# Optimization experiments

Measured on AMD Instinct MI355X. Metric: run time of the kernel, lower is better.

## Reference

```python
import jax, jax.numpy as jnp
import numpy as np

B, S, QD, VD, H = 32, 2048, 1024, 1024, 1024
NEG = -1e9


def setup_inputs() -> dict:
    key = jax.random.key(0)
    ks = jax.random.split(key, 7)
    query = jax.random.normal(ks[0], (B, QD), dtype=jnp.float32)
    value = jax.random.normal(ks[1], (B, S, VD), dtype=jnp.float32)
    mask = jax.random.randint(ks[2], (B, S), 0, 2).astype(bool)
    # params (Linear weights stored as [in, out] for einsum convenience)
    Wq = jax.random.normal(ks[3], (QD, H), dtype=jnp.float32) / np.sqrt(QD)
    bq = jax.random.normal(ks[4], (H,), dtype=jnp.float32) * 0.01
    Wv = jax.random.normal(ks[5], (VD, H), dtype=jnp.float32) / np.sqrt(VD)
    w = jax.random.normal(ks[6], (H,), dtype=jnp.float32) / np.sqrt(H)
    return {"query": query, "value": value, "mask": mask,
            "Wq": Wq, "bq": bq, "Wv": Wv, "w": w}


def reference(query, value, mask, Wq, bq, Wv, w):
    # q-projection: [B, H]
    hq = query @ Wq + bq
    # v-projection: [B, S, H]
    hv = jnp.einsum('bsv,vh->bsh', value, Wv)
    # additive attention energies: [B, S]
    logits = jnp.einsum('bsh,h->bs', jnp.tanh(hq[:, None, :] + hv), w)
    logits = jnp.where(mask, logits, NEG)
    return jax.nn.softmax(logits, axis=-1)
```

## Files before the change

### kernel.cpp

```cpp
#include <hip/hip_runtime.h>
#include <hip/hip_bf16.h>
#include <hip/hip_fp16.h>

typedef _Float16 f16;
typedef _Float16 f16x8 __attribute__((ext_vector_type(8)));
typedef float f32x16 __attribute__((ext_vector_type(16)));
typedef unsigned int u32;

#define BB 32
#define SS 2048
#define HH 1024
#define KK 1024

#define WS_BP 0
#define WS_HQ (2u*1024u*1024u)
#define WS_LP (WS_HQ + 131072u)

__device__ __forceinline__ float tanh_f(float x) {
    float e = __expf(2.0f * x);
    return 1.0f - 2.0f * __builtin_amdgcn_rcpf(e + 1.0f);
}

__device__ __forceinline__ void write_a16(char* dst, int off, float4 va, float4 vb) {
    union { f16 h[8]; uint4 u; } pk;
    pk.h[0] = (f16)va.x; pk.h[1] = (f16)va.y; pk.h[2] = (f16)va.z; pk.h[3] = (f16)va.w;
    pk.h[4] = (f16)vb.x; pk.h[5] = (f16)vb.y; pk.h[6] = (f16)vb.z; pk.h[7] = (f16)vb.w;
    *(uint4*)(dst + off) = pk.u;
}

__global__ void pack_wv(const float* __restrict__ Wv, f16* __restrict__ BP) {
    int i = blockIdx.x * 256 + threadIdx.x;
    int k = i >> 10, n = i & 1023;
    float v = Wv[i];
    int ntb = n >> 8, wc = (n >> 6) & 3, ntl = (n >> 5) & 1, nl = n & 31;
    int kit = k >> 5, ks = (k >> 4) & 1, lg = (k >> 3) & 1, j = k & 7;
    int lane = lg * 32 + nl;
    BP[((((((ntb * 32 + kit) * 4 + wc) * 2 + ks) * 2 + ntl) * 64 + lane) * 8) + j] = (f16)v;
}

__global__ void hq_kernel(const float* __restrict__ query, const float* __restrict__ Wq,
                          const float* __restrict__ bq, float* __restrict__ hq) {
    int b = blockIdx.y;
    int h = (blockIdx.x & 3) * 256 + threadIdx.x;
    int v0 = (blockIdx.x >> 2) * 256;
    float acc = 0.f;
#pragma unroll 8
    for (int v = 0; v < 256; ++v)
        acc += query[b * 1024 + v0 + v] * Wq[(v0 + v) * 1024 + h];
    if (v0 == 0) acc += bq[h];
    atomicAdd(&hq[b * 1024 + h], acc);
}

__launch_bounds__(256, 3)
__global__ void fused_main(const float* __restrict__ value, const f16* __restrict__ BP,
                           const float* __restrict__ hq, const float* __restrict__ wvec,
                           float* __restrict__ lpart) {
    __shared__ char A0[4096];
    __shared__ char A1[4096];
    __shared__ float part[256];

    int bid = blockIdx.x;
    int tile = (bid & 7) * 512 + (bid >> 3);
    int Mt = tile >> 2, ntb = tile & 3;
    int m0 = Mt << 6;
    int b = m0 >> 11, s0 = m0 & 2047;

    int tid = threadIdx.x;
    int wc = tid >> 6, l = tid & 63;
    int l31 = l & 31, lg = l >> 5;

    int arow = tid >> 2;
    const float* aga = value + (size_t)(m0 + arow) * 1024 + (tid & 3) * 8;
    int aw = ((arow >> 5) * 2 + ((tid & 3) >> 1)) * 1024
           + ((((tid & 3) & 1) << 5) + (arow & 31)) * 16;

    const char* bg = (const char*)BP + (size_t)ntb * 524288 + (size_t)wc * 4096
                   + (size_t)l * 16;

    int a_off0 = l * 16;
    int a_off1 = 2048 + l * 16;

    const f32x16 fzero = {};
    f32x16 acc[2][2];
#pragma unroll
    for (int mt = 0; mt < 2; ++mt)
#pragma unroll
        for (int nt = 0; nt < 2; ++nt) acc[mt][nt] = fzero;

    f16x8 bvA[4], bvB[4];
    float4 fe0, fe1, fo0, fo1;

#define COMPUTE(Ab, BV) do { \
        f16x8 a00 = *(const f16x8*)((Ab) + a_off0); \
        f16x8 a10 = *(const f16x8*)((Ab) + a_off1); \
        f16x8 a01 = *(const f16x8*)((Ab) + a_off0 + 1024); \
        f16x8 a11 = *(const f16x8*)((Ab) + a_off1 + 1024); \
        __builtin_amdgcn_s_setprio(1); \
        acc[0][0] = __builtin_amdgcn_mfma_f32_32x32x16_f16(a00, (BV)[0], acc[0][0], 0, 0, 0); \
        acc[0][1] = __builtin_amdgcn_mfma_f32_32x32x16_f16(a00, (BV)[1], acc[0][1], 0, 0, 0); \
        acc[1][0] = __builtin_amdgcn_mfma_f32_32x32x16_f16(a10, (BV)[0], acc[1][0], 0, 0, 0); \
        acc[1][1] = __builtin_amdgcn_mfma_f32_32x32x16_f16(a10, (BV)[1], acc[1][1], 0, 0, 0); \
        acc[0][0] = __builtin_amdgcn_mfma_f32_32x32x16_f16(a01, (BV)[2], acc[0][0], 0, 0, 0); \
        acc[0][1] = __builtin_amdgcn_mfma_f32_32x32x16_f16(a01, (BV)[3], acc[0][1], 0, 0, 0); \
        acc[1][0] = __builtin_amdgcn_mfma_f32_32x32x16_f16(a11, (BV)[2], acc[1][0], 0, 0, 0); \
        acc[1][1] = __builtin_amdgcn_mfma_f32_32x32x16_f16(a11, (BV)[3], acc[1][1], 0, 0, 0); \
        __builtin_amdgcn_s_setprio(0); \
    } while (0)

#define LOADB(BV, e) do { \
        const char* bt_ = bg + (size_t)(e) * 16384; \
        (BV)[0] = *(const f16x8*)(bt_); \
        (BV)[1] = *(const f16x8*)(bt_ + 1024); \
        (BV)[2] = *(const f16x8*)(bt_ + 2048); \
        (BV)[3] = *(const f16x8*)(bt_ + 3072); \
    } while (0)

    {
        const float4* ap = (const float4*)aga;
        float4 p0 = ap[0], p1 = ap[1];
        write_a16(A0, aw, p0, p1);
        const float4* ap1 = (const float4*)(aga + 32);
        fo0 = ap1[0]; fo1 = ap1[1];
        LOADB(bvA, 0);
        asm volatile("s_waitcnt lgkmcnt(0)" ::: "memory");
        __builtin_amdgcn_s_barrier();
    }

#pragma unroll 1
    for (int tt = 0; tt < 16; ++tt) {
        {
            LOADB(bvB, 2 * tt + 1);
            int xa = 2 * tt + 2; if (xa > 31) xa = 31;
            const float4* ap = (const float4*)(aga + xa * 32);
            fe0 = ap[0]; fe1 = ap[1];
            COMPUTE(A0, bvA);
            write_a16(A1, aw, fo0, fo1);
            asm volatile("s_waitcnt lgkmcnt(0)" ::: "memory");
            __builtin_amdgcn_s_barrier();
        }
        {
            int xb = 2 * tt + 2; if (xb > 31) xb = 31;
            LOADB(bvA, xb);
            int xc = 2 * tt + 3; if (xc > 31) xc = 31;
            const float4* ap = (const float4*)(aga + xc * 32);
            fo0 = ap[0]; fo1 = ap[1];
            COMPUTE(A1, bvB);
            if (tt < 15) write_a16(A0, aw, fe0, fe1);
            asm volatile("s_waitcnt lgkmcnt(0)" ::: "memory");
            __builtin_amdgcn_s_barrier();
        }
    }
#undef COMPUTE
#undef LOADB

    int h0 = ntb * 256 + wc * 64 + l31;
    int h1 = h0 + 32;
    float hq0 = hq[b * 1024 + h0], hq1 = hq[b * 1024 + h1];
    float w0 = wvec[h0], w1 = wvec[h1];

#pragma unroll
    for (int mt = 0; mt < 2; ++mt) {
#pragma unroll
        for (int i = 0; i < 8; ++i) {
            float pa = tanh_f(hq0 + acc[mt][0][2 * i]) * w0
                     + tanh_f(hq1 + acc[mt][1][2 * i]) * w1;
            float pb = tanh_f(hq0 + acc[mt][0][2 * i + 1]) * w0
                     + tanh_f(hq1 + acc[mt][1][2 * i + 1]) * w1;
            float ea = __shfl_xor(pa, 1), eb = __shfl_xor(pb, 1);
            float g = (l & 1) ? (pb + eb) : (pa + ea);
            g += __shfl_xor(g, 2); g += __shfl_xor(g, 4);
            g += __shfl_xor(g, 8); g += __shfl_xor(g, 16);
            if (l31 < 2) {
                int r = 2 * i + (l31 & 1);
                int row = mt * 32 + (r & 3) + ((r >> 2) << 3) + (lg << 2);
                part[wc * 64 + row] = g;
            }
        }
    }
    __syncthreads();
    if (tid < 64) {
        float s = part[tid] + part[64 + tid] + part[128 + tid] + part[192 + tid];
        lpart[((size_t)ntb * 32 + b) * 2048 + s0 + tid] = s;
    }
}

__global__ void softmax_kernel(const float* __restrict__ lp, const int* __restrict__ mask,
                               float* __restrict__ out) {
    __shared__ float redm[16];
    __shared__ float reds[16];
    const int P = 32 * 2048;
    int b = blockIdx.x, t = threadIdx.x;
    int wid = t >> 6, lane = t & 63;
    int i0 = b * 2048 + t, i1 = i0 + 1024;
    float l0 = lp[i0] + lp[P + i0] + lp[2 * P + i0] + lp[3 * P + i0];
    float l1 = lp[i1] + lp[P + i1] + lp[2 * P + i1] + lp[3 * P + i1];
    float a0 = mask[i0] ? l0 : -1e9f;
    float a1 = mask[i1] ? l1 : -1e9f;
    float mx = fmaxf(a0, a1);
#pragma unroll
    for (int off = 1; off < 64; off <<= 1) mx = fmaxf(mx, __shfl_xor(mx, off));
    if (lane == 0) redm[wid] = mx;
    __syncthreads();
    mx = redm[0];
#pragma unroll
    for (int i = 1; i < 16; ++i) mx = fmaxf(mx, redm[i]);
    float e0 = __expf(a0 - mx), e1 = __expf(a1 - mx);
    float s = e0 + e1;
#pragma unroll
    for (int off = 1; off < 64; off <<= 1) s += __shfl_xor(s, off);
    if (lane == 0) reds[wid] = s;
    __syncthreads();
    float tot = 0.f;
#pragma unroll
    for (int i = 0; i < 16; ++i) tot += reds[i];
    float inv = 1.0f / tot;
    out[b * 2048 + t] = e0 * inv;
    out[b * 2048 + 1024 + t] = e1 * inv;
}

extern "C" void kernel_launch(void* const* d_in, const int* in_sizes, int n_in,
                              void* d_out, int out_size, void* d_ws, size_t ws_size,
                              hipStream_t stream) {
    const float* query = (const float*)d_in[0];
    const float* value = (const float*)d_in[1];
    const int*   mask  = (const int*)d_in[2];
    const float* Wq    = (const float*)d_in[3];
    const float* bq    = (const float*)d_in[4];
    const float* Wv    = (const float*)d_in[5];
    const float* wv    = (const float*)d_in[6];

    char* ws = (char*)d_ws;
    f16*   BP    = (f16*)(ws + WS_BP);
    float* hq    = (float*)(ws + WS_HQ);
    float* lpart = (float*)(ws + WS_LP);
    float* out   = (float*)d_out;

    (void)hipMemsetAsync(hq, 0, BB * HH * sizeof(float), stream);
    pack_wv<<<(KK * HH) / 256, 256, 0, stream>>>(Wv, BP);
    hq_kernel<<<dim3(16, BB), 256, 0, stream>>>(query, Wq, bq, hq);
    fused_main<<<4096, 256, 0, stream>>>(value, BP, hq, wv, lpart);
    softmax_kernel<<<BB, 1024, 0, stream>>>(lpart, mask, out);
}
```

Baseline: 223.6 us.

## Double K-step per stage to 64 and halve barriers in main GEMM loop

Widens each pipeline stage from 32 to 64 K elements by repacking Wv to match, doubling the LDS A buffers, and loading four float4s of value per thread per iteration. The loop runs 16 stages with one barrier each instead of 32, and the B fragment loads are interleaved between the two compute halves. The aim is to cut barrier and loop overhead and give each stage more MFMA work to hide global load latency. In exchange it uses more LDS, which may lower occupancy, and more registers, and the next stage's B fragments are loaded after compute, which may leave their latency exposed.

```diff
diff --git a/kernel.cpp b/kernel.cpp
--- a/kernel.cpp
+++ b/kernel.cpp
@@ -33,9 +33,9 @@
     int k = i >> 10, n = i & 1023;
     float v = Wv[i];
     int ntb = n >> 8, wc = (n >> 6) & 3, ntl = (n >> 5) & 1, nl = n & 31;
-    int kit = k >> 5, ks = (k >> 4) & 1, lg = (k >> 3) & 1, j = k & 7;
+    int kit = k >> 6, ks = (k >> 4) & 3, lg = (k >> 3) & 1, j = k & 7;
     int lane = lg * 32 + nl;
-    BP[((((((ntb * 32 + kit) * 4 + wc) * 2 + ks) * 2 + ntl) * 64 + lane) * 8) + j] = (f16)v;
+    BP[((((((ntb * 16 + kit) * 4 + wc) * 4 + ks) * 2 + ntl) * 64 + lane) * 8) + j] = (f16)v;
 }
 
 __global__ void hq_kernel(const float* __restrict__ query, const float* __restrict__ Wq,
@@ -55,8 +55,8 @@
 __global__ void fused_main(const float* __restrict__ value, const f16* __restrict__ BP,
                            const float* __restrict__ hq, const float* __restrict__ wvec,
                            float* __restrict__ lpart) {
-    __shared__ char A0[4096];
-    __shared__ char A1[4096];
+    __shared__ char A0[8192];
+    __shared__ char A1[8192];
     __shared__ float part[256];
 
     int bid = blockIdx.x;
@@ -70,15 +70,15 @@
     int l31 = l & 31, lg = l >> 5;
 
     int arow = tid >> 2;
-    const float* aga = value + (size_t)(m0 + arow) * 1024 + (tid & 3) * 8;
-    int aw = ((arow >> 5) * 2 + ((tid & 3) >> 1)) * 1024
-           + ((((tid & 3) & 1) << 5) + (arow & 31)) * 16;
-
-    const char* bg = (const char*)BP + (size_t)ntb * 524288 + (size_t)wc * 4096
+    const float* aga = value + (size_t)(m0 + arow) * 1024 + (tid & 3) * 16;
+    int aw0 = ((arow >> 5) * 4 + (tid & 3)) * 1024 + ((arow & 31) << 4);
+    int aw1 = aw0 + 512;
+
+    const char* bg = (const char*)BP + (size_t)ntb * 524288 + (size_t)wc * 8192
                    + (size_t)l * 16;
 
-    int a_off0 = l * 16;
-    int a_off1 = 2048 + l * 16;
+    int a_m0 = l * 16;
+    int a_m1 = 4096 + l * 16;
 
     const f32x16 fzero = {};
     f32x16 acc[2][2];
@@ -88,13 +88,13 @@
         for (int nt = 0; nt < 2; ++nt) acc[mt][nt] = fzero;
 
     f16x8 bvA[4], bvB[4];
-    float4 fe0, fe1, fo0, fo1;
-
-#define COMPUTE(Ab, BV) do { \
-        f16x8 a00 = *(const f16x8*)((Ab) + a_off0); \
-        f16x8 a10 = *(const f16x8*)((Ab) + a_off1); \
-        f16x8 a01 = *(const f16x8*)((Ab) + a_off0 + 1024); \
-        f16x8 a11 = *(const f16x8*)((Ab) + a_off1 + 1024); \
+    float4 ar0, ar1, ar2, ar3;
+
+#define COMPUTE_HALF(Ab, BV, kso) do { \
+        f16x8 a00 = *(const f16x8*)((Ab) + a_m0 + ((kso) + 0) * 1024); \
+        f16x8 a10 = *(const f16x8*)((Ab) + a_m1 + ((kso) + 0) * 1024); \
+        f16x8 a01 = *(const f16x8*)((Ab) + a_m0 + ((kso) + 1) * 1024); \
+        f16x8 a11 = *(const f16x8*)((Ab) + a_m1 + ((kso) + 1) * 1024); \
         __builtin_amdgcn_s_setprio(1); \
         acc[0][0] = __builtin_amdgcn_mfma_f32_32x32x16_f16(a00, (BV)[0], acc[0][0], 0, 0, 0); \
         acc[0][1] = __builtin_amdgcn_mfma_f32_32x32x16_f16(a00, (BV)[1], acc[0][1], 0, 0, 0); \
@@ -107,8 +107,8 @@
         __builtin_amdgcn_s_setprio(0); \
     } while (0)
 
-#define LOADB(BV, e) do { \
-        const char* bt_ = bg + (size_t)(e) * 16384; \
+#define LOADB(BV, e, half) do { \
+        const char* bt_ = bg + (size_t)(e) * 32768 + (half) * 4096; \
         (BV)[0] = *(const f16x8*)(bt_); \
         (BV)[1] = *(const f16x8*)(bt_ + 1024); \
         (BV)[2] = *(const f16x8*)(bt_ + 2048); \
@@ -117,40 +117,35 @@
 
     {
         const float4* ap = (const float4*)aga;
-        float4 p0 = ap[0], p1 = ap[1];
-        write_a16(A0, aw, p0, p1);
-        const float4* ap1 = (const float4*)(aga + 32);
-        fo0 = ap1[0]; fo1 = ap1[1];
-        LOADB(bvA, 0);
+        ar0 = ap[0]; ar1 = ap[1]; ar2 = ap[2]; ar3 = ap[3];
+        write_a16(A0, aw0, ar0, ar1);
+        write_a16(A0, aw1, ar2, ar3);
+        LOADB(bvA, 0, 0);
+        LOADB(bvB, 0, 1);
         asm volatile("s_waitcnt lgkmcnt(0)" ::: "memory");
         __builtin_amdgcn_s_barrier();
     }
 
 #pragma unroll 1
-    for (int tt = 0; tt < 16; ++tt) {
-        {
-            LOADB(bvB, 2 * tt + 1);
-            int xa = 2 * tt + 2; if (xa > 31) xa = 31;
-            const float4* ap = (const float4*)(aga + xa * 32);
-            fe0 = ap[0]; fe1 = ap[1];
-            COMPUTE(A0, bvA);
-            write_a16(A1, aw, fo0, fo1);
-            asm volatile("s_waitcnt lgkmcnt(0)" ::: "memory");
-            __builtin_amdgcn_s_barrier();
-        }
-        {
-            int xb = 2 * tt + 2; if (xb > 31) xb = 31;
-            LOADB(bvA, xb);
-            int xc = 2 * tt + 3; if (xc > 31) xc = 31;
-            const float4* ap = (const float4*)(aga + xc * 32);
-            fo0 = ap[0]; fo1 = ap[1];
-            COMPUTE(A1, bvB);
-            if (tt < 15) write_a16(A0, aw, fe0, fe1);
-            asm volatile("s_waitcnt lgkmcnt(0)" ::: "memory");
-            __builtin_amdgcn_s_barrier();
-        }
-    }
-#undef COMPUTE
+    for (int e = 0; e < 16; ++e) {
+        char* Ac = (e & 1) ? A1 : A0;
+        char* An = (e & 1) ? A0 : A1;
+        int en = (e < 15) ? e + 1 : 15;
+
+        const float4* ap = (const float4*)(aga + en * 64);
+        ar0 = ap[0]; ar1 = ap[1]; ar2 = ap[2]; ar3 = ap[3];
+
+        COMPUTE_HALF(Ac, bvA, 0);
+        LOADB(bvA, en, 0);
+        COMPUTE_HALF(Ac, bvB, 2);
+        LOADB(bvB, en, 1);
+
+        write_a16(An, aw0, ar0, ar1);
+        write_a16(An, aw1, ar2, ar3);
+        asm volatile("s_waitcnt lgkmcnt(0)" ::: "memory");
+        __builtin_amdgcn_s_barrier();
+    }
+#undef COMPUTE_HALF
 #undef LOADB
 
     int h0 = ntb * 256 + wc * 64 + l31;
```

Result: no change. 221.2 us (-1.1%).
